# Optimization experiments

Measured on AMD Instinct MI355X. Metric: run time of the kernel, lower is better.

The kernel has to match this reference:

```python
import jax, jax.numpy as jnp
import numpy as np

B, H, W = 16, 16, 16
DIM = 768
NH = 8
HD = DIM // NH
NEXP = 8
TOPK = 2
DSTATE = 1
DTRANK = 4
KDIR = 4


def setup_inputs() -> dict:
    key = jax.random.key(0)
    ks = jax.random.split(key, 16)
    s = 1.0 / float(np.sqrt(DIM))
    inp = {
        'x': jax.random.normal(ks[0], (B, H, W, DIM)),
        'sa_in_w': jax.random.normal(ks[1], (3 * DIM, DIM)) * s,
        'sa_in_b': jnp.zeros((3 * DIM,)),
        'sa_out_w': jax.random.normal(ks[2], (DIM, DIM)) * s,
        'sa_out_b': jnp.zeros((DIM,)),
        'ca_in_w': jax.random.normal(ks[3], (2 * DIM, DIM)) * s,
        'ca_in_b': jnp.zeros((2 * DIM,)),
        'expert_queries': jax.random.normal(ks[4], (NEXP, DIM)) * s,
        'e_in_w': jax.random.normal(ks[5], (NEXP, 2 * DIM, DIM)) * s,
        'e_in_b': jnp.zeros((NEXP, 2 * DIM)),
        'e_conv_w': jax.random.normal(ks[6], (NEXP, DIM, 1, 3, 3)) / 3.0,
        'e_conv_b': jnp.zeros((NEXP, DIM)),
        'e_xproj_w': jax.random.normal(ks[7], (NEXP, KDIR, DTRANK + 2 * DSTATE, DIM)) * s,
        'e_dtproj_w': jax.random.normal(ks[8], (NEXP, KDIR, DIM, DTRANK)) * 0.1,
        'e_dtproj_b': jax.random.uniform(ks[9], (NEXP, KDIR, DIM), minval=-4.0, maxval=-2.0),
        'e_Alog': jax.random.uniform(ks[10], (NEXP, KDIR, DIM, DSTATE), minval=0.0, maxval=1.0),
        'e_D': jnp.ones((NEXP, KDIR, DIM)),
        'e_ln_scale': jnp.ones((NEXP, DIM)),
        'e_ln_bias': jnp.zeros((NEXP, DIM)),
    }
    return {k: v.astype(jnp.float32) for k, v in inp.items()}


def _selective_scan(xs, Wx, Wdt, bdt, Alog, D):
    # xs: [B, L, d]; Wx: [R+2N, d]; Wdt: [d, R]; Alog: [d, N]; D: [d]
    dbl = jnp.einsum('bld,ed->ble', xs, Wx)
    dt = jax.nn.softplus(jnp.einsum('blr,dr->bld', dbl[..., :DTRANK], Wdt) + bdt)
    Bm = dbl[..., DTRANK:DTRANK + DSTATE]
    Cm = dbl[..., DTRANK + DSTATE:]
    A = -jnp.exp(Alog)  # [d, N]

    def step(h, t):
        dt_t, B_t, C_t, x_t = t  # [b,d],[b,N],[b,N],[b,d]
        h = jnp.exp(dt_t[:, :, None] * A) * h + (dt_t * x_t)[:, :, None] * B_t[:, None, :]
        return h, jnp.einsum('bdn,bn->bd', h, C_t)

    b, L, d = xs.shape
    h0 = jnp.zeros((b, d, DSTATE), xs.dtype)
    tm = lambda a: jnp.moveaxis(a, 1, 0)
    _, ys = jax.lax.scan(step, h0, (tm(dt), tm(Bm), tm(Cm), tm(xs)))
    return jnp.moveaxis(ys, 0, 1) + D * xs


def _expert(in_w, in_b, conv_w, conv_b, xproj_w, dtp_w, dtp_b, Alog, D, ln_s, ln_b, x):
    b = x.shape[0]
    xz = jnp.einsum('bhwc,oc->bhwo', x, in_w) + in_b
    xc, z = jnp.split(xz, 2, axis=-1)
    xn = jax.lax.conv_general_dilated(jnp.transpose(xc, (0, 3, 1, 2)), conv_w,
                                      (1, 1), ((1, 1), (1, 1)), feature_group_count=DIM)
    xc = jax.nn.silu(jnp.transpose(xn + conv_b[None, :, None, None], (0, 2, 3, 1)))
    L = H * W
    xh = xc.reshape(b, L, DIM)                              # row-major 'h'
    xv = jnp.transpose(xc, (0, 2, 1, 3)).reshape(b, L, DIM)  # col-major 'v'
    seqs = jnp.stack([xh, xh[:, ::-1], xv, xv[:, ::-1]])     # [4, b, L, d]
    ys = jax.vmap(_selective_scan)(seqs, xproj_w, dtp_w, dtp_b, Alog, D)
    yv = ys[2] + ys[3][:, ::-1]
    yv = jnp.transpose(yv.reshape(b, W, H, DIM), (0, 2, 1, 3)).reshape(b, L, DIM)
    y = (ys[0] + ys[1][:, ::-1] + yv).reshape(b, H, W, DIM)
    mu = y.mean(-1, keepdims=True)
    var = ((y - mu) ** 2).mean(-1, keepdims=True)
    y = (y - mu) * jax.lax.rsqrt(var + 1e-5) * ln_s + ln_b   # out_norm (LayerNorm)
    y = y * jax.nn.silu(z)
    return y.mean((1, 2))  # AdaptiveAvgPool2d((1,1)) -> [b, DIM]


def _forward(x, sa_in_w, sa_in_b, sa_out_w, sa_out_b, ca_in_w, ca_in_b, expert_queries,
             e_in_w, e_in_b, e_conv_w, e_conv_b, e_xproj_w, e_dtproj_w, e_dtproj_b,
             e_Alog, e_D, e_ln_scale, e_ln_bias):
    b = x.shape[0]
    L = H * W
    scale = 1.0 / float(np.sqrt(HD))
    xs = x.reshape(b, L, DIM)
    # spatial self-attention (eval mode: dropout off)
    qkv = xs @ sa_in_w.T + sa_in_b
    q, k, v = [a.reshape(b, L, NH, HD) for a in jnp.split(qkv, 3, -1)]
    att = jax.nn.softmax(jnp.einsum('bqhd,bkhd->bhqk', q, k) * scale, -1)
    ctx = jnp.einsum('bhqk,bkhd->bqhd', att, v).reshape(b, L, DIM) @ sa_out_w.T + sa_out_b
    # expert cross-attention: only head-averaged attention weights are used
    q2 = (ctx @ ca_in_w[:DIM].T + ca_in_b[:DIM]).reshape(b, L, NH, HD)
    k2 = (expert_queries @ ca_in_w[DIM:].T + ca_in_b[DIM:]).reshape(NEXP, NH, HD)
    aw = jax.nn.softmax(jnp.einsum('blhd,ehd->bhle', q2, k2) * scale, -1).mean(1)  # [b,L,E]
    gate = jax.nn.softmax(aw.mean(1), -1)  # [b, E]
    tk_scores, tk_idx = jax.lax.top_k(gate, TOPK)
    wgt = jax.nn.softmax(tk_scores, -1)
    # dense expert compute (all experts on all samples), then gather top-k
    all_out = jax.vmap(_expert, in_axes=(0,) * 11 + (None,))(
        e_in_w, e_in_b, e_conv_w, e_conv_b, e_xproj_w, e_dtproj_w, e_dtproj_b,
        e_Alog, e_D, e_ln_scale, e_ln_bias, x)  # [E, b, DIM]
    per_b = jnp.transpose(all_out, (1, 0, 2))  # [b, E, DIM]
    sel = jnp.take_along_axis(per_b, tk_idx[:, :, None], axis=1)  # [b, K, DIM]
    return jnp.sum(wgt[:, :, None] * sel, axis=1)  # [b, DIM]


def reference(x, sa_in_w, sa_in_b, sa_out_w, sa_out_b, ca_in_w, ca_in_b, expert_queries,
              e_in_w, e_in_b, e_conv_w, e_conv_b, e_xproj_w, e_dtproj_w, e_dtproj_b,
              e_Alog, e_D, e_ln_scale, e_ln_bias):
    return _forward(x, sa_in_w, sa_in_b, sa_out_w, sa_out_b, ca_in_w, ca_in_b, expert_queries,
                    e_in_w, e_in_b, e_conv_w, e_conv_b, e_xproj_w, e_dtproj_w, e_dtproj_b,
                    e_Alog, e_D, e_ln_scale, e_ln_bias)
```

## Files before the change

kernel.cpp:

```cpp
#include <hip/hip_runtime.h>
#include <hip/hip_bf16.h>


#define LTOK 256
#define DIMC 768

typedef unsigned short ushortt;
typedef __attribute__((ext_vector_type(8))) short bf16x8;
typedef __attribute__((ext_vector_type(4))) float f32x4;

#define LOG2E 1.44269504f
#define LN2   0.69314718f

__device__ __forceinline__ float fexp2(float x) { return __builtin_amdgcn_exp2f(x); }
__device__ __forceinline__ float flog2(float x) { return __builtin_amdgcn_logf(x); }

__device__ __forceinline__ ushortt f2b(float f) {
  union { float f; unsigned u; } c; c.f = f;
  unsigned r = (c.u + 0x7FFFu + ((c.u >> 16) & 1u)) >> 16;
  return (ushortt)r;
}

__global__ __launch_bounds__(256) void mk_mcast4(
    const float* __restrict__ s0, ushortt* __restrict__ d0,
    const float* __restrict__ s1, ushortt* __restrict__ d1,
    const float* __restrict__ s2, ushortt* __restrict__ d2,
    const float* __restrict__ s3, ushortt* __restrict__ d3)
{
  long g = (long)blockIdx.x * 256 + threadIdx.x;
  const float* s; ushortt* dst; long o;
  if (g < 786432)       { s = s0; dst = d0; o = g; }
  else if (g < 1228800) { s = s1; dst = d1; o = g - 786432; }
  else if (g < 1376256) { s = s2; dst = d2; o = g - 1228800; }
  else                  { s = s3; dst = d3; o = g - 1376256; }
  o <<= 2;
  float4 v = *(const float4*)(s + o);
  ushort4 w;
  w.x = f2b(v.x); w.y = f2b(v.y); w.z = f2b(v.z); w.w = f2b(v.w);
  *(ushort4*)(dst + o) = w;
}

__global__ __launch_bounds__(256) void mk_cast(const float* __restrict__ in,
                                               ushortt* __restrict__ outp, long n)
{
  long i = ((long)blockIdx.x * 256 + threadIdx.x) * 4;
  if (i + 3 < n) {
    float4 v = *(const float4*)(in + i);
    ushort4 o;
    o.x = f2b(v.x); o.y = f2b(v.y); o.z = f2b(v.z); o.w = f2b(v.w);
    *(ushort4*)(outp + i) = o;
  }
}

__global__ __launch_bounds__(256) void mk_mfma(
    const ushortt* __restrict__ A, const ushortt* __restrict__ B,
    const float* __restrict__ bias, void* __restrict__ C,
    int K, int lda, int ldb, int ldc,
    int zdiv, long sA1, long sA2, long sB1, long sB2, long sC1, long sC2,
    long sBias,
    const int* __restrict__ pairExp, int tilesN,
    int outBf, int splitN, void* __restrict__ C2, int ldc2, int outBf2, int c2vt)
{
  int z = blockIdx.y;
  long aoff, boff, coff, biasoff = 0;
  if (pairExp) {
    int e = pairExp[z];
    aoff = (long)(z >> 1) * sA1; boff = (long)e * sB1;
    coff = (long)z * sC1; biasoff = (long)e * sBias;
  } else {
    int z1 = z / zdiv, z2 = z - z1 * zdiv;
    aoff = (long)z1 * sA1 + (long)z2 * sA2;
    boff = (long)z1 * sB1 + (long)z2 * sB2;
    coff = (long)z1 * sC1 + (long)z2 * sC2;
  }
  int tile = blockIdx.x;
  int tm = tile / tilesN, tn = tile - tm * tilesN;
  long m0 = (long)tm << 7, n0 = (long)tn << 7;

  __shared__ ushortt As[128][40];
  __shared__ ushortt Bs[128][40];

  int tid = threadIdx.x;
  int lane = tid & 63, wvi = tid >> 6;
  int wr = wvi >> 1, wc = wvi & 1;
  int lm = lane & 15, lg = lane >> 4;

  f32x4 zero4 = {0.f, 0.f, 0.f, 0.f};
  f32x4 acc[4][4];
#pragma unroll
  for (int i = 0; i < 4; i++)
#pragma unroll
    for (int j = 0; j < 4; j++) acc[i][j] = zero4;

  const ushortt* Ab = A + aoff;
  const ushortt* Bb = B + boff;

  for (int k0 = 0; k0 < K; k0 += 32) {
#pragma unroll
    for (int h = 0; h < 2; h++) {
      int q = tid + h * 256;
      int row = q >> 2, ck = (q & 3) << 3;
      *(uint4*)&As[row][ck] = *(const uint4*)(Ab + (m0 + row) * lda + k0 + ck);
      *(uint4*)&Bs[row][ck] = *(const uint4*)(Bb + (n0 + row) * ldb + k0 + ck);
    }
    __syncthreads();
    bf16x8 af[4], bfr[4];
#pragma unroll
    for (int i = 0; i < 4; i++)
      af[i] = *(const bf16x8*)&As[wr * 64 + i * 16 + lm][lg << 3];
#pragma unroll
    for (int j = 0; j < 4; j++)
      bfr[j] = *(const bf16x8*)&Bs[wc * 64 + j * 16 + lm][lg << 3];
#pragma unroll
    for (int i = 0; i < 4; i++)
#pragma unroll
      for (int j = 0; j < 4; j++)
        acc[i][j] = __builtin_amdgcn_mfma_f32_16x16x32_bf16(af[i], bfr[j], acc[i][j], 0, 0, 0);
    __syncthreads();
  }

#pragma unroll
  for (int mt = 0; mt < 4; mt++) {
#pragma unroll
    for (int nt = 0; nt < 4; nt++) {
      long grow = m0 + wr * 64 + mt * 16 + lg * 4;
      long gcol = n0 + wc * 64 + nt * 16 + lm;
      float bv = bias ? bias[biasoff + gcol] : 0.f;
      if ((int)gcol < splitN) {
#pragma unroll
        for (int r = 0; r < 4; r++) {
          float v = acc[mt][nt][r] + bv;
          long idx = coff + (grow + r) * ldc + gcol;
          if (outBf) ((ushortt*)C)[idx] = f2b(v);
          else ((float*)C)[idx] = v;
        }
      } else if (c2vt) {
        int cc = (int)gcol - splitN;
        int hh = cc / 96, jj = cc - hh * 96;
#pragma unroll
        for (int r = 0; r < 4; r++) {
          float v = acc[mt][nt][r] + bv;
          long gr = grow + r;
          long b = gr >> 8, t = gr & 255;
          long idx = (((b * 8 + hh) * 128 + jj) << 8) + t;
          ((ushortt*)C2)[idx] = f2b(v);
        }
      } else {
        long col = gcol - splitN;
#pragma unroll
        for (int r = 0; r < 4; r++) {
          float v = acc[mt][nt][r] + bv;
          long idx = coff + (grow + r) * ldc2 + col;
          if (outBf2) ((ushortt*)C2)[idx] = f2b(v);
          else ((float*)C2)[idx] = v;
        }
      }
    }
  }
}

__global__ __launch_bounds__(256) void mk_gemm(
    const float* __restrict__ A, const float* __restrict__ B,
    const float* __restrict__ bias, float* __restrict__ C,
    int M, int N, int K, int lda, int ldb, int ldc, int tilesN)
{
  int tile = blockIdx.x;
  int tm = tile / tilesN, tn = tile - tm * tilesN;
  int m0 = tm << 6, n0 = tn << 6;

  __shared__ float As[16][68];
  __shared__ float Bs[16][68];

  int tid = threadIdx.x;
  int tx = tid & 15, ty = tid >> 4;
  int lrow = tid >> 2;
  int lk = (tid & 3) << 2;

  float acc[4][4];
#pragma unroll
  for (int i = 0; i < 4; i++)
#pragma unroll
    for (int j = 0; j < 4; j++) acc[i][j] = 0.f;

  for (int k0 = 0; k0 < K; k0 += 16) {
    {
      int gm = m0 + lrow;
      float4 v = {0.f, 0.f, 0.f, 0.f};
      if (gm < M) v = *(const float4*)(A + (long)gm * lda + (k0 + lk));
      As[lk + 0][lrow] = v.x; As[lk + 1][lrow] = v.y;
      As[lk + 2][lrow] = v.z; As[lk + 3][lrow] = v.w;
    }
    {
      int gn = n0 + lrow;
      float4 v = {0.f, 0.f, 0.f, 0.f};
      if (gn < N) v = *(const float4*)(B + (long)gn * ldb + (k0 + lk));
      Bs[lk + 0][lrow] = v.x; Bs[lk + 1][lrow] = v.y;
      Bs[lk + 2][lrow] = v.z; Bs[lk + 3][lrow] = v.w;
    }
    __syncthreads();
#pragma unroll
    for (int kk = 0; kk < 16; kk++) {
      float4 a = *(const float4*)&As[kk][ty << 2];
      float4 b = *(const float4*)&Bs[kk][tx << 2];
      acc[0][0] += a.x * b.x; acc[0][1] += a.x * b.y; acc[0][2] += a.x * b.z; acc[0][3] += a.x * b.w;
      acc[1][0] += a.y * b.x; acc[1][1] += a.y * b.y; acc[1][2] += a.y * b.z; acc[1][3] += a.y * b.w;
      acc[2][0] += a.z * b.x; acc[2][1] += a.z * b.y; acc[2][2] += a.z * b.z; acc[2][3] += a.z * b.w;
      acc[3][0] += a.w * b.x; acc[3][1] += a.w * b.y; acc[3][2] += a.w * b.z; acc[3][3] += a.w * b.w;
    }
    __syncthreads();
  }

#pragma unroll
  for (int i = 0; i < 4; i++) {
    int gm = m0 + (ty << 2) + i;
    if (gm >= M) continue;
#pragma unroll
    for (int j = 0; j < 4; j++) {
      int gn = n0 + (tx << 2) + j;
      if (gn >= N) continue;
      float v = acc[i][j];
      if (bias) v += bias[gn];
      C[(long)gm * ldc + gn] = v;
    }
  }
}

__global__ __launch_bounds__(256) void mk_softmax(const float* __restrict__ scores,
                                                  ushortt* __restrict__ att, float scale)
{
  int row = (blockIdx.x << 2) + (threadIdx.x >> 6);
  int lane = threadIdx.x & 63;
  const float* p = scores + (long)row * 256 + (lane << 2);
  float4 v = *(const float4*)p;
  float m = fmaxf(fmaxf(v.x, v.y), fmaxf(v.z, v.w));
#pragma unroll
  for (int o = 32; o; o >>= 1) m = fmaxf(m, __shfl_xor(m, o, 64));
  float sl = scale * LOG2E;
  v.x = fexp2(sl * (v.x - m));
  v.y = fexp2(sl * (v.y - m));
  v.z = fexp2(sl * (v.z - m));
  v.w = fexp2(sl * (v.w - m));
  float s = v.x + v.y + v.z + v.w;
#pragma unroll
  for (int o = 32; o; o >>= 1) s += __shfl_xor(s, o, 64);
  float r = 1.f / s;
  ushort4 o4;
  o4.x = f2b(v.x * r); o4.y = f2b(v.y * r); o4.z = f2b(v.z * r); o4.w = f2b(v.w * r);
  *(ushort4*)(att + (long)row * 256 + (lane << 2)) = o4;
}

__global__ __launch_bounds__(256) void mk_gates(const float* __restrict__ q2,
                                                const float* __restrict__ k2,
                                                float* __restrict__ gacc)
{
  __shared__ float k2p[8 * 808];
  int b = blockIdx.x >> 4, q = blockIdx.x & 15;
  for (int i = threadIdx.x; i < 6144; i += 256) {
    int e = i / 768, rem = i - e * 768;
    int h = rem / 96, j = rem - h * 96;
    k2p[e * 808 + h * 100 + j] = k2[i];
  }
  __syncthreads();
  const float scale = 0.10206207261596577f;
  int wid = threadIdx.x >> 6, lane = threadIdx.x & 63;
  int h = lane >> 3, e = lane & 7;
  const float* kp = &k2p[e * 808 + h * 100];
  float accL = 0.f;
#pragma unroll
  for (int ti = 0; ti < 4; ti++) {
    int l = q * 16 + wid * 4 + ti;
    const float* qh = q2 + ((long)b * LTOK + l) * DIMC + h * 96;
    float sum = 0.f;
#pragma unroll
    for (int j = 0; j < 96; j += 4) {
      float4 qv = *(const float4*)(qh + j);
      float4 kv = *(const float4*)(kp + j);
      sum += qv.x * kv.x + qv.y * kv.y + qv.z * kv.z + qv.w * kv.w;
    }
    float s = sum * scale;
    float mx = s;
#pragma unroll
    for (int o = 1; o <= 4; o <<= 1) mx = fmaxf(mx, __shfl_xor(mx, o, 64));
    float ex = fexp2((s - mx) * LOG2E);
    float se = ex;
#pragma unroll
    for (int o = 1; o <= 4; o <<= 1) se += __shfl_xor(se, o, 64);
    accL += ex / se;
  }
#pragma unroll
  for (int o = 8; o <= 32; o <<= 1) accL += __shfl_xor(accL, o, 64);
  __shared__ float red[4][8];
  if (lane < 8) red[wid][lane] = accL;
  __syncthreads();
  if (threadIdx.x < 8) {
    float v = red[0][threadIdx.x] + red[1][threadIdx.x] +
              red[2][threadIdx.x] + red[3][threadIdx.x];
    atomicAdd(&gacc[b * 8 + threadIdx.x], v);
  }
}

__global__ __launch_bounds__(64) void mk_gatetop(const float* __restrict__ gacc,
                                                 int* __restrict__ pe,
                                                 float* __restrict__ pw)
{
  int b = threadIdx.x;
  if (b >= 16) return;
  float g[8];
  for (int e = 0; e < 8; e++) g[e] = gacc[b * 8 + e] * (1.f / (8.f * 256.f));
  float mx = g[0];
  for (int e = 1; e < 8; e++) mx = fmaxf(mx, g[e]);
  float se = 0.f;
  for (int e = 0; e < 8; e++) { g[e] = expf(g[e] - mx); se += g[e]; }
  for (int e = 0; e < 8; e++) g[e] /= se;
  int i0 = 0;
  for (int e = 1; e < 8; e++) if (g[e] > g[i0]) i0 = e;
  int i1 = (i0 == 0) ? 1 : 0;
  for (int e = 0; e < 8; e++) if (e != i0 && g[e] > g[i1]) i1 = e;
  float w0 = 1.f / (1.f + expf(g[i1] - g[i0]));
  pe[2 * b] = i0; pe[2 * b + 1] = i1;
  pw[2 * b] = w0; pw[2 * b + 1] = 1.f - w0;
}

__global__ __launch_bounds__(768) void mk_conv(const float* __restrict__ xzx,
                                               const float* __restrict__ cw,
                                               const float* __restrict__ cb,
                                               const int* __restrict__ pe,
                                               float* __restrict__ xc)
{
  int blk = blockIdx.x;
  int p = blk >> 8, t = blk & 255;
  int e = pe[p];
  int h = t >> 4, w = t & 15;
  int c = threadIdx.x;
  const float* wp = cw + ((long)e * DIMC + c) * 9;
  float acc = cb[e * DIMC + c];
#pragma unroll
  for (int dh = 0; dh < 3; dh++) {
    int hh = h + dh - 1;
    if (hh < 0 || hh > 15) continue;
#pragma unroll
    for (int dw = 0; dw < 3; dw++) {
      int ww = w + dw - 1;
      if (ww < 0 || ww > 15) continue;
      acc += xzx[((long)p * LTOK + hh * 16 + ww) * DIMC + c] * wp[dh * 3 + dw];
    }
  }
  xc[((long)p * LTOK + t) * DIMC + c] = acc / (1.f + fexp2(-acc * LOG2E));
}

__device__ __forceinline__ int tmap(int dir, int s) {
  if (dir == 0) return s;
  if (dir == 1) return 255 - s;
  if (dir == 2) return ((s & 15) << 4) | (s >> 4);
  int u = 255 - s;
  return ((u & 15) << 4) | (u >> 4);
}

__global__ __launch_bounds__(256) void mk_dbl(const float* __restrict__ xc,
                                              const float* __restrict__ xproj,
                                              const int* __restrict__ pe,
                                              float* __restrict__ dblm)
{
  int p = blockIdx.x >> 6;
  int tq = blockIdx.x & 63;
  int wid = threadIdx.x >> 6, lane = threadIdx.x & 63;
  int m = tq * 4 + wid;
  int e = pe[p];
  const float* xr = xc + ((long)p * LTOK + m) * DIMC;
  const float* wb = xproj + (long)e * 24 * DIMC;
  float4 xv[3];
#pragma unroll
  for (int j = 0; j < 3; j++) xv[j] = *(const float4*)(xr + j * 256 + lane * 4);
  float acc[24];
#pragma unroll
  for (int r = 0; r < 24; r++) {
    const float* wr = wb + r * DIMC;
    float s = 0.f;
#pragma unroll
    for (int j = 0; j < 3; j++) {
      float4 wv = *(const float4*)(wr + j * 256 + lane * 4);
      s += xv[j].x * wv.x + xv[j].y * wv.y + xv[j].z * wv.z + xv[j].w * wv.w;
    }
    acc[r] = s;
  }
#pragma unroll
  for (int r = 0; r < 24; r++)
#pragma unroll
    for (int o = 32; o; o >>= 1) acc[r] += __shfl_xor(acc[r], o, 64);
  if (lane == 0) {
    float* o = dblm + (long)p * 6144;
#pragma unroll
    for (int dd = 0; dd < 4; dd++) {
      int s = tmap(dd, m);
      int ss = ((s & 31) << 3) | (s >> 5);
      float* oa = o + dd * 1024 + ss * 4;
      oa[0] = acc[dd * 6 + 0]; oa[1] = acc[dd * 6 + 1];
      oa[2] = acc[dd * 6 + 2]; oa[3] = acc[dd * 6 + 3];
      float* ob = o + 4096 + dd * 512 + ss * 2;
      ob[0] = acc[dd * 6 + 4]; ob[1] = acc[dd * 6 + 5];
    }
  }
}

__global__ __launch_bounds__(512, 6) void mk_scan(const float* __restrict__ xc,
                                               const float* __restrict__ dblm,
                                               const float* __restrict__ dtw,
                                               const float* __restrict__ dtb,
                                               const float* __restrict__ Alog,
                                               const float* __restrict__ Dp,
                                               const int* __restrict__ pe,
                                               float* __restrict__ yac)
{
  __shared__ __attribute__((aligned(16))) float dtS[4096];
  __shared__ __attribute__((aligned(16))) float bcS[2048];
  __shared__ float yS[256 * 18];
  __shared__ float ahS[32][16][2];
  __shared__ float dsum[16];
  int blk = blockIdx.x;
  int p = blk / 48, cg = blk - p * 48;
  int c0 = cg << 4;
  int e = pe[p];
  int tid = threadIdx.x;
  {
    const float4* src = (const float4*)(dblm + (long)p * 6144);
    float4* dA = (float4*)dtS;
    for (int i = tid; i < 1024; i += 512) dA[i] = src[i];
    if (tid < 512) ((float4*)bcS)[tid] = src[1024 + tid];
  }
  for (int i = tid; i < 256 * 18; i += 512) yS[i] = 0.f;
  if (tid < 16) {
    float s = 0.f;
#pragma unroll
    for (int dd = 0; dd < 4; dd++) s += Dp[(long)(e * 4 + dd) * DIMC + c0 + tid];
    dsum[tid] = s;
  }
  __syncthreads();

  int c = tid & 15;
  int rr = tid >> 4;
  int seg = rr & 7;
  int dir = rr >> 3;
  int d = c0 + c;
  const float* xcp = xc + (long)p * LTOK * DIMC + d;
  long pb = (long)(e * 4 + dir) * DIMC + d;
  float4 wv = *(const float4*)(dtw + pb * 4);
  wv.x *= LOG2E; wv.y *= LOG2E; wv.z *= LOG2E; wv.w *= LOG2E;
  float bdt = dtb[pb] * LOG2E;
  float Ad = -fexp2(Alog[pb] * LOG2E);
  int t0 = seg << 5;
  const float* dtP = &dtS[(dir << 10) + (seg << 2)];
  const float* bcP = &bcS[(dir << 9) + (seg << 1)];

  float h = 0.f, ap = 1.f;
#pragma unroll 1
  for (int tb = 0; tb < 32; tb += 4) {
#pragma unroll
    for (int u = 0; u < 4; u++) {
      int i = tb + u;
      float4 dv = *(const float4*)(dtP + i * 32);
      float2 bc = *(const float2*)(bcP + i * 16);
      int mm = tmap(dir, t0 + i);
      float xv = xcp[(long)mm * DIMC];
      float xl = wv.x * dv.x + wv.y * dv.y + wv.z * dv.z + wv.w * dv.w + bdt;
      float te = fexp2(xl);
      float g = flog2(1.f + te);
      g = (xl > 86.f) ? xl : g;
      float de = fexp2(g * Ad);
      h = de * h + (g * LN2 * bc.x) * xv;
      ap *= de;
    }
    __builtin_amdgcn_sched_barrier(0);
  }
  ahS[rr][c][0] = ap;
  ahS[rr][c][1] = h;
  __syncthreads();

  float hh = 0.f;
  {
    int base = dir << 3;
    float av[8], hv[8];
#pragma unroll
    for (int j = 0; j < 8; j++) {
      av[j] = ahS[base + j][c][0];
      hv[j] = ahS[base + j][c][1];
    }
#pragma unroll
    for (int j = 0; j < 7; j++)
      if (j < seg) hh = av[j] * hh + hv[j];
  }

#pragma unroll 1
  for (int tb = 0; tb < 32; tb += 4) {
#pragma unroll
    for (int u = 0; u < 4; u++) {
      int i = tb + u;
      float4 dv = *(const float4*)(dtP + i * 32);
      float2 bc = *(const float2*)(bcP + i * 16);
      int mm = tmap(dir, t0 + i);
      float xv = xcp[(long)mm * DIMC];
      float xl = wv.x * dv.x + wv.y * dv.y + wv.z * dv.z + wv.w * dv.w + bdt;
      float te = fexp2(xl);
      float g = flog2(1.f + te);
      g = (xl > 86.f) ? xl : g;
      float de = fexp2(g * Ad);
      hh = de * hh + (g * LN2 * bc.x) * xv;
      atomicAdd(&yS[mm * 18 + c + (((mm >> 5) & 1) << 1)], hh * bc.y);
    }
    __builtin_amdgcn_sched_barrier(0);
  }
  __syncthreads();

  const float* xcb = xc + (long)p * LTOK * DIMC + c0;
  float* yp = yac + (long)p * LTOK * DIMC + c0;
  for (int i = tid; i < 4096; i += 512) {
    int t = i >> 4, cz = i & 15;
    yp[(long)t * DIMC + cz] = yS[t * 18 + cz + (((t >> 5) & 1) << 1)] +
        xcb[(long)t * DIMC + cz] * dsum[cz];
  }
}

__global__ __launch_bounds__(256) void mk_lnfin(const float* __restrict__ yac,
                                                const float* __restrict__ xzz,
                                                const float* __restrict__ lns,
                                                const float* __restrict__ lnb,
                                                const int* __restrict__ pe,
                                                float* __restrict__ eo)
{
  int blk = blockIdx.x;
  int p = blk >> 4, ts = blk & 15;
  int e = pe[p];
  int tid = threadIdx.x;
  int wid = tid >> 6, lane = tid & 63;
  float ls[12], lb[12], acc[12];
#pragma unroll
  for (int i = 0; i < 12; i++) {
    int d = i * 64 + lane;
    ls[i] = lns[e * DIMC + d];
    lb[i] = lnb[e * DIMC + d];
    acc[i] = 0.f;
  }
#pragma unroll
  for (int tt = 0; tt < 4; tt++) {
    int t = ts * 16 + wid * 4 + tt;
    const float* yr = yac + ((long)p * LTOK + t) * DIMC;
    const float* zr = xzz + ((long)p * LTOK + t) * DIMC;
    float v[12];
    float s = 0.f;
#pragma unroll
    for (int i = 0; i < 12; i++) { v[i] = yr[i * 64 + lane]; s += v[i]; }
#pragma unroll
    for (int o = 32; o; o >>= 1) s += __shfl_xor(s, o, 64);
    float mu = s * (1.f / 768.f);
    float sq = 0.f;
#pragma unroll
    for (int i = 0; i < 12; i++) { float dlt = v[i] - mu; sq += dlt * dlt; }
#pragma unroll
    for (int o = 32; o; o >>= 1) sq += __shfl_xor(sq, o, 64);
    float rs = rsqrtf(sq * (1.f / 768.f) + 1e-5f);
#pragma unroll
    for (int i = 0; i < 12; i++) {
      float y = (v[i] - mu) * rs * ls[i] + lb[i];
      float z = zr[i * 64 + lane];
      y *= z / (1.f + fexp2(-z * LOG2E));
      acc[i] += y;
    }
  }
  __shared__ float sacc[768];
  for (int j = tid; j < 768; j += 256) sacc[j] = 0.f;
  __syncthreads();
#pragma unroll
  for (int i = 0; i < 12; i++) atomicAdd(&sacc[i * 64 + lane], acc[i]);
  __syncthreads();
  for (int j = tid; j < 768; j += 256) atomicAdd(&eo[(long)p * DIMC + j], sacc[j]);
}

__global__ __launch_bounds__(768) void mk_out(const float* __restrict__ eo,
                                              const float* __restrict__ pw,
                                              float* __restrict__ out)
{
  int b = blockIdx.x, d = threadIdx.x;
  float v = pw[2 * b] * eo[(long)(2 * b) * DIMC + d] +
            pw[2 * b + 1] * eo[(long)(2 * b + 1) * DIMC + d];
  out[b * DIMC + d] = v * (1.f / 256.f);
}

extern "C" void kernel_launch(void* const* d_in, const int* in_sizes, int n_in,
                              void* d_out, int out_size, void* d_ws, size_t ws_size,
                              hipStream_t stream)
{
  const float* x        = (const float*)d_in[0];
  const float* sa_in_w  = (const float*)d_in[1];
  const float* sa_in_b  = (const float*)d_in[2];
  const float* sa_out_w = (const float*)d_in[3];
  const float* sa_out_b = (const float*)d_in[4];
  const float* ca_in_w  = (const float*)d_in[5];
  const float* ca_in_b  = (const float*)d_in[6];
  const float* eq       = (const float*)d_in[7];
  const float* e_in_w   = (const float*)d_in[8];
  const float* e_in_b   = (const float*)d_in[9];
  const float* e_conv_w = (const float*)d_in[10];
  const float* e_conv_b = (const float*)d_in[11];
  const float* e_xproj  = (const float*)d_in[12];
  const float* e_dtw    = (const float*)d_in[13];
  const float* e_dtb    = (const float*)d_in[14];
  const float* e_Alog   = (const float*)d_in[15];
  const float* e_D      = (const float*)d_in[16];
  const float* e_lns    = (const float*)d_in[17];
  const float* e_lnb    = (const float*)d_in[18];
  float* out = (float*)d_out;

  float* ws = (float*)d_ws;
  ushortt* qk_b   = (ushortt*)(ws + 0);
  float*   scores = ws + 6291456;
  ushortt* dump_b = (ushortt*)(ws + 6291456);
  ushortt* ctxa_b = (ushortt*)(ws + 7864320);
  ushortt* att_b  = (ushortt*)(ws + 14680064);
  ushortt* vt_b   = (ushortt*)(ws + 18874368);
  ushortt* xb     = (ushortt*)(ws + 20971520);
  ushortt* wqkv_b = (ushortt*)(ws + 22544384);
  ushortt* saow_b = (ushortt*)(ws + 23429120);
  ushortt* caw_b  = (ushortt*)(ws + 23724032);
  ushortt* ctx_b  = (ushortt*)(ws + 0);
  float*   q2     = ws + 1572864;
  float*   k2     = ws + 25165824;
  int*     pe     = (int*)(ws + 25171968);
  float*   pw     = ws + 25172000;
  float*   eo     = ws + 25172032;
  float*   gacc   = ws + 25393216;
  float*   xz_x   = ws + 0;
  float*   xz_z   = ws + 6291456;
  ushortt* ew_b   = (ushortt*)(ws + 12582912);
  float*   xc     = ws + 12582912;
  float*   yac    = ws + 18874368;
  float*   dblm   = ws + 0;

  const float scale = 0.10206207261596577f;

  mk_mcast4<<<5952, 256, 0, stream>>>(x, xb, sa_in_w, wqkv_b, sa_out_w, saow_b,
                                      ca_in_w, caw_b);
  mk_mfma<<<dim3(576, 1), 256, 0, stream>>>(xb, wqkv_b, sa_in_b, qk_b,
      768, 768, 768, 1536, 1, 0, 0, 0, 0, 0, 0, 0, nullptr, 18,
      1, 1536, vt_b, 0, 1, 1);
  mk_mfma<<<dim3(4, 128), 256, 0, stream>>>(qk_b, qk_b + 768, nullptr, scores,
      96, 1536, 1536, 256, 8, 393216, 96, 393216, 96, 524288, 65536, 0, nullptr, 2,
      0, 1 << 30, nullptr, 0, 0, 0);
  mk_softmax<<<8192, 256, 0, stream>>>(scores, att_b, scale);
  mk_mfma<<<dim3(2, 128), 256, 0, stream>>>(att_b, vt_b, nullptr, ctxa_b,
      256, 256, 256, 768, 8, 524288, 65536, 262144, 32768, 196608, 96, 0, nullptr, 1,
      1, 96, dump_b, 32, 1, 0);
  mk_cast<<<9216, 256, 0, stream>>>(e_in_w, ew_b, 9437184);
  mk_mfma<<<dim3(192, 1), 256, 0, stream>>>(ctxa_b, saow_b, sa_out_b, ctx_b,
      768, 768, 768, 768, 1, 0, 0, 0, 0, 0, 0, 0, nullptr, 6,
      1, 1 << 30, nullptr, 0, 0, 0);
  mk_mfma<<<dim3(192, 1), 256, 0, stream>>>(ctx_b, caw_b, ca_in_b, q2,
      768, 768, 768, 768, 1, 0, 0, 0, 0, 0, 0, 0, nullptr, 6,
      0, 1 << 30, nullptr, 0, 0, 0);
  mk_gemm<<<dim3(12, 1), 256, 0, stream>>>(eq, ca_in_w + 589824, ca_in_b + 768, k2,
      8, 768, 768, 768, 768, 768, 12);
  (void)hipMemsetAsync(gacc, 0, 128 * sizeof(float), stream);
  (void)hipMemsetAsync(eo, 0, 24576 * sizeof(float), stream);
  mk_gates<<<256, 256, 0, stream>>>(q2, k2, gacc);
  mk_gatetop<<<1, 64, 0, stream>>>(gacc, pe, pw);
  mk_mfma<<<dim3(24, 32), 256, 0, stream>>>(xb, ew_b, e_in_b, xz_x,
      768, 768, 768, 768, 1, 196608, 0, 1179648, 0, 196608, 0, 1536, pe, 12,
      0, 768, xz_z, 768, 0, 0);
  mk_conv<<<32 * 256, 768, 0, stream>>>(xz_x, e_conv_w, e_conv_b, pe, xc);
  mk_dbl<<<2048, 256, 0, stream>>>(xc, e_xproj, pe, dblm);
  mk_scan<<<1536, 512, 0, stream>>>(xc, dblm, e_dtw, e_dtb, e_Alog, e_D, pe, yac);
  mk_lnfin<<<512, 256, 0, stream>>>(yac, xz_z, e_lns, e_lnb, pe, eo);
  mk_out<<<16, 768, 0, stream>>>(eo, pw, out);

  (void)in_sizes; (void)n_in; (void)out_size; (void)ws_size;
}
```

Measured before the change: 629.1 us.

## Load GEMM tiles directly into LDS via global_load_lds with XOR swizzle

Replaces the register-staged global-to-shared copies in the bf16 MFMA GEMM with direct global_load_lds 16-byte transfers. The padded LDS tiles become unpadded tiles with an XOR swizzle, applied on both write and read, to avoid bank conflicts. Fragment addresses are precomputed outside the k-loop. This aims to cut VGPR traffic and instruction count on tile loads, but relies on the swizzle and per-wave lane layout of the LDS-direct load being correct.

```diff
diff --git a/kernel.cpp b/kernel.cpp
--- a/kernel.cpp
+++ b/kernel.cpp
@@ -11,6 +11,12 @@
 
 #define LOG2E 1.44269504f
 #define LN2   0.69314718f
+
+__device__ __forceinline__ void gld16(const ushortt* gp, ushortt* lp) {
+  __builtin_amdgcn_global_load_lds(
+      (const __attribute__((address_space(1))) void*)gp,
+      (__attribute__((address_space(3))) void*)lp, 16, 0, 0);
+}
 
 __device__ __forceinline__ float fexp2(float x) { return __builtin_amdgcn_exp2f(x); }
 __device__ __forceinline__ float flog2(float x) { return __builtin_amdgcn_logf(x); }
@@ -77,8 +83,8 @@
   int tm = tile / tilesN, tn = tile - tm * tilesN;
   long m0 = (long)tm << 7, n0 = (long)tn << 7;
 
-  __shared__ ushortt As[128][40];
-  __shared__ ushortt Bs[128][40];
+  __shared__ ushortt As[128 * 32];
+  __shared__ ushortt Bs[128 * 32];
 
   int tid = threadIdx.x;
   int lane = tid & 63, wvi = tid >> 6;
@@ -95,22 +101,37 @@
   const ushortt* Ab = A + aoff;
   const ushortt* Bb = B + boff;
 
+  int srow = (wvi << 5) + (lane >> 2);
+  int sglog = ((lane & 3) ^ ((lane >> 3) & 3)) << 3;
+  const ushortt* agp = Ab + (m0 + srow) * lda + sglog;
+  const ushortt* bgp = Bb + (n0 + srow) * ldb + sglog;
+  ushortt* al0 = &As[(wvi << 5) << 5];
+  ushortt* al1 = &As[((wvi << 5) + 16) << 5];
+  ushortt* bl0 = &Bs[(wvi << 5) << 5];
+  ushortt* bl1 = &Bs[((wvi << 5) + 16) << 5];
+
+  int pswz = (lg ^ ((lm >> 1) & 3)) << 3;
+  const ushortt* afp[4];
+  const ushortt* bfp[4];
+#pragma unroll
+  for (int i = 0; i < 4; i++) {
+    afp[i] = &As[((wr * 64 + i * 16 + lm) << 5) + pswz];
+    bfp[i] = &Bs[((wc * 64 + i * 16 + lm) << 5) + pswz];
+  }
+
   for (int k0 = 0; k0 < K; k0 += 32) {
-#pragma unroll
-    for (int h = 0; h < 2; h++) {
-      int q = tid + h * 256;
-      int row = q >> 2, ck = (q & 3) << 3;
-      *(uint4*)&As[row][ck] = *(const uint4*)(Ab + (m0 + row) * lda + k0 + ck);
-      *(uint4*)&Bs[row][ck] = *(const uint4*)(Bb + (n0 + row) * ldb + k0 + ck);
-    }
+    gld16(agp, al0);
+    gld16(agp + 16 * lda, al1);
+    gld16(bgp, bl0);
+    gld16(bgp + 16 * ldb, bl1);
+    agp += 32; bgp += 32;
     __syncthreads();
     bf16x8 af[4], bfr[4];
 #pragma unroll
-    for (int i = 0; i < 4; i++)
-      af[i] = *(const bf16x8*)&As[wr * 64 + i * 16 + lm][lg << 3];
-#pragma unroll
-    for (int j = 0; j < 4; j++)
-      bfr[j] = *(const bf16x8*)&Bs[wc * 64 + j * 16 + lm][lg << 3];
+    for (int i = 0; i < 4; i++) {
+      af[i] = *(const bf16x8*)afp[i];
+      bfr[i] = *(const bf16x8*)bfp[i];
+    }
 #pragma unroll
     for (int i = 0; i < 4; i++)
 #pragma unroll
```

New measurement: 622.4 us. About the same (-1.1%).
